# Performance work log

Measured on AMD Instinct MI355X. Metric: run time of the kernel, lower is better.

## Reference

```python
import jax, jax.numpy as jnp
import numpy as np

ALPHA = 0.5
TEMP = 0.1
TEMP2 = 0.05  # hardcoded in nt_xent_loss2
NUM_CLASSES = 10
EPS = 1e-12


def setup_inputs() -> dict:
    key = jax.random.key(0)
    k1, k2, k3 = jax.random.split(key, 3)
    B, D, C = 4096, 256, NUM_CLASSES
    cls_feats = jax.random.normal(k1, (B, D), dtype=jnp.float32)
    predicts = jax.random.normal(k2, (B, C), dtype=jnp.float32)
    targets = jax.random.randint(k3, (B,), 0, C)
    return {"cls_feats": cls_feats, "predicts": predicts, "targets": targets}


def _nt_xent_loss(feats, labels):
    B = feats.shape[0]
    eye = jnp.eye(B, dtype=bool)
    same = labels[:, None] == labels[None, :]
    mask = (same & ~eye).astype(feats.dtype)            # positives, no diagonal
    s = jnp.einsum('bd,cd->bc', feats, feats) / TEMP     # [B,B]
    s = jnp.where(eye, 0.0, s)                           # subtract diag_embed(diag)
    logits = s - jax.lax.stop_gradient(jnp.max(s, axis=1, keepdims=True))
    log_denom = jnp.log(jnp.sum(jnp.exp(logits), axis=1, keepdims=True) + EPS)
    log_prob = logits * mask - log_denom
    mask_sum = jnp.sum(mask, axis=1)
    mask_sum = jnp.where(mask_sum == 0, 1.0, mask_sum)
    pos_logits = jnp.sum(mask * log_prob, axis=1) / mask_sum
    return -jnp.mean(pos_logits)


def _nt_xent_loss2(feats, labels):
    B = feats.shape[0]
    eye = jnp.eye(B, dtype=bool)
    same = labels[:, None] == labels[None, :]
    mask = (same & ~eye).astype(feats.dtype)
    diff = ~same                                         # mask2 / different-label pairs
    S = (feats @ feats.T) / TEMP2                        # [B,B]
    val = jnp.where(diff, S, 0.0)                        # dot * different_label_mask

    # The torch loop body depends only on labels[i] -> compute once per class.
    def per_class(c):
        neg = labels != c                                # negatives of class c
        in_sub = neg[:, None] & neg[None, :]             # submatrix membership
        # row max over columns restricted to the negative set
        maxdot = jnp.max(jnp.where(neg[None, :], val, -jnp.inf), axis=1)  # [B]
        shifted = jnp.where(in_sub, val - maxdot[:, None], -jnp.inf)
        s_c = jnp.sum(jnp.exp(shifted))                  # exp_terms.sum()
        n_c = jnp.sum(jnp.where(in_sub, diff, False).astype(jnp.float32))
        return s_c, n_c

    sums, counts = jax.lax.map(jax.checkpoint(per_class), jnp.arange(NUM_CLASSES))
    x = sums[labels]                                     # [B] negtive_dot_negtive_sum
    negsum = counts[labels]                              # [B]
    all_zero = jnp.all(negsum == 0)
    x = jnp.where(all_zero, x, x / negsum)
    log_prob_row = -jnp.log(x + EPS)                     # constant across each row
    mask_sum = jnp.sum(mask, axis=1)
    mask_sum_safe = jnp.where(mask_sum == 0, 1.0, mask_sum)
    pos_logits = (mask_sum * log_prob_row) / mask_sum_safe
    return -jnp.mean(pos_logits)


def reference(cls_feats, predicts, targets):
    norm = jnp.maximum(jnp.linalg.norm(cls_feats, axis=-1, keepdims=True), EPS)
    feats = cls_feats / norm                             # F.normalize(dim=-1)
    logp = jax.nn.log_softmax(predicts, axis=-1)
    ce = -jnp.mean(jnp.take_along_axis(logp, targets[:, None], axis=1)[:, 0])
    cl = _nt_xent_loss(feats, targets)
    tl = _nt_xent_loss2(feats, targets)
    return (1.0 - ALPHA) * ce + ALPHA * cl + 0.5 * ALPHA * tl
```

## Files before the change

kernel.cpp:

```cpp
#include <hip/hip_runtime.h>
#include <math.h>

#define B 4096
#define D 256
#define NC 10
#define ZERO4 22528

typedef __attribute__((ext_vector_type(8))) short bf16x8;
typedef __attribute__((ext_vector_type(4))) float f32x4;

__device__ __forceinline__ unsigned short f2bf(float x) {
    unsigned int u = __float_as_uint(x);
    u += 0x7FFFu + ((u >> 16) & 1u);
    return (unsigned short)(u >> 16);
}

__device__ __forceinline__ float sel4f(float a, float b, float c, float d, int k) {
    float x = (k == 1) ? b : a;
    x = (k == 2) ? c : x;
    return (k == 3) ? d : x;
}
__device__ __forceinline__ int sel4i(int a, int b, int c, int d, int k) {
    int x = (k == 1) ? b : a;
    x = (k == 2) ? c : x;
    return (k == 3) ? d : x;
}

__global__ void prep_kernel(const float* __restrict__ pred, const int* __restrict__ tg,
                            float4* __restrict__ bigz, int* __restrict__ h,
                            float* __restrict__ scal) {
    __shared__ int histL[16];
    const int t = threadIdx.x, w = t >> 6, l = t & 63;
    const int r0 = blockIdx.x * 16;
    if (t < 16) histL[t] = 0;
    __syncthreads();
    int zi = blockIdx.x * 256 + t;
    if (zi < ZERO4) bigz[zi] = (float4){0.f, 0.f, 0.f, 0.f};

    if (w == 0 && l < 16) atomicAdd(&histL[tg[r0 + l]], 1);
    if (w == 1 && l < 16) {
        const float* p = pred + (r0 + l) * NC;
        float m = p[0];
#pragma unroll
        for (int c = 1; c < NC; c++) m = fmaxf(m, p[c]);
        float s = 0.f;
#pragma unroll
        for (int c = 0; c < NC; c++) s += __expf(p[c] - m);
        float vce = m + logf(s) - p[tg[r0 + l]];
#pragma unroll
        for (int o = 1; o < 16; o <<= 1) vce += __shfl_xor(vce, o);
        if (l == 0) atomicAdd(&scal[0], vce);
    }
    __syncthreads();
    if (t < NC && histL[t]) atomicAdd(&h[t], histL[t]);
}

__global__ void scatter_kernel(const float* __restrict__ feats, const int* __restrict__ tg,
                               const int* __restrict__ h, int* __restrict__ ccnt,
                               int* __restrict__ labelP, unsigned short* __restrict__ fP) {
    __shared__ int cb[16];
    __shared__ int wcnt[4][16];
    __shared__ int wabs[4][16];
    __shared__ int posS[256];
    const int t = threadIdx.x, w = t >> 6, l = t & 63;
    const int r0 = blockIdx.x * 256;
    if (t == 0) {
        int s = 0;
        for (int cc = 0; cc < NC; cc++) { cb[cc] = s; s += h[cc]; }
    }
    if (t < 256) {
        const int c = tg[r0 + t];
        unsigned long long below = (l == 0) ? 0ull : ((~0ull) >> (64 - l));
        int rank = 0;
#pragma unroll
        for (int cc = 0; cc < NC; cc++) {
            unsigned long long m = __ballot(c == cc);
            if (c == cc) rank = __popcll(m & below);
            if (l == 0) wcnt[w][cc] = __popcll(m);
        }
        __syncthreads();
        if (t < NC) {
            int pre[4], s = 0;
#pragma unroll
            for (int ww = 0; ww < 4; ww++) { pre[ww] = s; s += wcnt[ww][t]; }
            int b = cb[t] + atomicAdd(&ccnt[t], s);
#pragma unroll
            for (int ww = 0; ww < 4; ww++) wabs[ww][t] = b + pre[ww];
        }
        __syncthreads();
        int pos = wabs[w][c] + rank;
        labelP[pos] = c;
        posS[t] = pos;
    } else {
        __syncthreads();
        __syncthreads();
    }
    __syncthreads();

    const int gid = t >> 4, lg = t & 15;
#pragma unroll
    for (int it = 0; it < 4; ++it) {
        const int r = it * 64 + gid;
        float4 v[4];
#pragma unroll
        for (int k = 0; k < 4; k++) v[k] = ((const float4*)feats)[(r0 + r) * 64 + lg * 4 + k];
        float ss = 0.f;
#pragma unroll
        for (int k = 0; k < 4; k++)
            ss += v[k].x * v[k].x + v[k].y * v[k].y + v[k].z * v[k].z + v[k].w * v[k].w;
#pragma unroll
        for (int o = 1; o < 16; o <<= 1) ss += __shfl_xor(ss, o);
        float inv = 1.0f / fmaxf(sqrtf(ss), 1e-12f);
        bf16x8 o0, o1;
#pragma unroll
        for (int k = 0; k < 4; k++) {
            const float* vp = (const float*)&v[k];
            if (k < 2) {
#pragma unroll
                for (int e = 0; e < 4; e++) o0[k * 4 + e] = (short)f2bf(vp[e] * inv);
            } else {
#pragma unroll
                for (int e = 0; e < 4; e++) o1[(k - 2) * 4 + e] = (short)f2bf(vp[e] * inv);
            }
        }
        const int dst = posS[r];
        ((bf16x8*)fP)[dst * 32 + lg * 2 + 0] = o0;
        ((bf16x8*)fP)[dst * 32 + lg * 2 + 1] = o1;
    }
}

__launch_bounds__(256)
__global__ void gemm_kernel(const unsigned short* __restrict__ fP,
                            const int* __restrict__ labP,
                            float* __restrict__ E1, float* __restrict__ P1,
                            float* __restrict__ E2G, int* __restrict__ M2K) {
    __shared__ int labS[256];
    __shared__ int labR[32];

    const int t = threadIdx.x;
    const int w = t >> 6, l = t & 63;
    const int qr = l >> 4, lm = l & 15;
    const int row0 = blockIdx.x * 32;
    const int colB = blockIdx.y * 256;

    labS[t] = labP[colB + t];
    if (t < 32) labR[t] = labP[row0 + t];

    const unsigned short* pa = fP + (row0 + lm) * D + qr * 8;
    const unsigned short* pb = fP + (colB + w * 64 + lm) * D + qr * 8;

    f32x4 acc[2][4];
#pragma unroll
    for (int mb = 0; mb < 2; mb++)
#pragma unroll
        for (int nb = 0; nb < 4; nb++) acc[mb][nb] = (f32x4){0.f, 0.f, 0.f, 0.f};

#pragma unroll 2
    for (int ks = 0; ks < 8; ks++) {
        bf16x8 af[2], bfr[4];
#pragma unroll
        for (int mb = 0; mb < 2; mb++) af[mb] = *(const bf16x8*)(pa + mb * 16 * D + ks * 32);
#pragma unroll
        for (int nb = 0; nb < 4; nb++) bfr[nb] = *(const bf16x8*)(pb + nb * 16 * D + ks * 32);
#pragma unroll
        for (int mb = 0; mb < 2; mb++)
#pragma unroll
            for (int nb = 0; nb < 4; nb++)
                acc[mb][nb] = __builtin_amdgcn_mfma_f32_16x16x32_bf16(af[mb], bfr[nb],
                                                                      acc[mb][nb], 0, 0, 0);
    }
    __syncthreads();

    const int cA = labS[w * 64];
    const int cB = labS[w * 64 + 63];
    const bool split = (cA != cB);
    int cj[4];
#pragma unroll
    for (int nb = 0; nb < 4; nb++) cj[nb] = labS[w * 64 + nb * 16 + lm];
    int liR[2][4];
#pragma unroll
    for (int mb = 0; mb < 2; mb++)
#pragma unroll
        for (int r = 0; r < 4; r++) liR[mb][r] = labR[mb * 16 + qr * 4 + r];

    float e1p[2][4], p1p[2][4], e2a[2][4], e2b[2][4];
    int kpa[2][4], kpb[2][4];
#pragma unroll
    for (int mb = 0; mb < 2; mb++)
#pragma unroll
        for (int r = 0; r < 4; r++) {
            e1p[mb][r] = 0.f; p1p[mb][r] = 0.f;
            e2a[mb][r] = 0.f; e2b[mb][r] = 0.f;
            kpa[mb][r] = 0; kpb[mb][r] = 0;
        }

#pragma unroll
    for (int mb = 0; mb < 2; mb++)
#pragma unroll
        for (int nb = 0; nb < 4; nb++) {
            const bool isA = (cj[nb] == cA);
#pragma unroll
            for (int r = 0; r < 4; r++) {
                float g = acc[mb][nb][r];
                int R = row0 + mb * 16 + qr * 4 + r;
                int C = colB + w * 64 + nb * 16 + lm;
                float s1 = (R == C) ? 0.f : 10.f * g;
                float e1 = __expf(s1);
                float e2 = e1 * e1;
                int key = __float_as_int(20.f * g + 64.f);
                e1p[mb][r] += e1;
                p1p[mb][r] += (cj[nb] == liR[mb][r]) ? s1 : 0.f;
                e2a[mb][r] += isA ? e2 : 0.f;
                e2b[mb][r] += isA ? 0.f : e2;
                kpa[mb][r] = isA ? max(kpa[mb][r], key) : kpa[mb][r];
                kpb[mb][r] = isA ? kpb[mb][r] : max(kpb[mb][r], key);
            }
        }

#pragma unroll
    for (int mb = 0; mb < 2; mb++) {
#pragma unroll
        for (int r = 0; r < 4; r++) {
#pragma unroll
            for (int off = 1; off < 16; off <<= 1) {
                e1p[mb][r] += __shfl_xor(e1p[mb][r], off);
                p1p[mb][r] += __shfl_xor(p1p[mb][r], off);
                e2a[mb][r] += __shfl_xor(e2a[mb][r], off);
                kpa[mb][r] = max(kpa[mb][r], __shfl_xor(kpa[mb][r], off));
            }
            if (split) {
#pragma unroll
                for (int off = 1; off < 16; off <<= 1) {
                    e2b[mb][r] += __shfl_xor(e2b[mb][r], off);
                    kpb[mb][r] = max(kpb[mb][r], __shfl_xor(kpb[mb][r], off));
                }
            }
        }
        if (lm < 4) {
            const int row = row0 + mb * 16 + qr * 4 + lm;
            atomicAdd(&E1[row], sel4f(e1p[mb][0], e1p[mb][1], e1p[mb][2], e1p[mb][3], lm));
            atomicAdd(&P1[row], sel4f(p1p[mb][0], p1p[mb][1], p1p[mb][2], p1p[mb][3], lm));
            atomicAdd(&E2G[row * NC + cA],
                      sel4f(e2a[mb][0], e2a[mb][1], e2a[mb][2], e2a[mb][3], lm));
            atomicMax(&M2K[row * NC + cA],
                      sel4i(kpa[mb][0], kpa[mb][1], kpa[mb][2], kpa[mb][3], lm));
            if (split) {
                atomicAdd(&E2G[row * NC + cB],
                          sel4f(e2b[mb][0], e2b[mb][1], e2b[mb][2], e2b[mb][3], lm));
                atomicMax(&M2K[row * NC + cB],
                          sel4i(kpb[mb][0], kpb[mb][1], kpb[mb][2], kpb[mb][3], lm));
            }
        }
    }
}

__global__ void rowfin_kernel(const int* __restrict__ labP, const int* __restrict__ h,
                              const float* __restrict__ E1, const float* __restrict__ P1,
                              const float* __restrict__ E2G, const int* __restrict__ M2K,
                              float* __restrict__ sums, float* __restrict__ scal,
                              int* __restrict__ done, float* __restrict__ out) {
    __shared__ float ssumL[16];
    __shared__ int lastS;
    const int t = threadIdx.x;
    if (t < 16) ssumL[t] = 0.f;
    __syncthreads();
    const int i = blockIdx.x * 64 + t;
    const int li = labP[i];
    float E2[NC], M2[NC];
#pragma unroll
    for (int k = 0; k < NC; k++) {
        E2[k] = E2G[i * NC + k];
        int key = M2K[i * NC + k];
        M2[k] = (key > 0) ? (__int_as_float(key) - 64.f) : -3.0e38f;
    }
    const int hl = h[li];
    E2[li] = (float)hl;
    M2[li] = 0.f;
    float m1 = -3.0e38f, m2 = -3.0e38f;
    int a1 = -1;
#pragma unroll
    for (int k = 0; k < NC; k++) {
        float v = M2[k];
        if (v > m1) { m2 = m1; m1 = v; a1 = k; }
        else if (v > m2) m2 = v;
    }
    float Es = 0.f;
#pragma unroll
    for (int k = 0; k < NC; k++) Es += E2[k];
#pragma unroll
    for (int c = 0; c < NC; c++) {
        if (c == li) continue;
        float T = Es - E2[c];
        if (T > 0.f) {
            float md = (a1 == c) ? m2 : m1;
            atomicAdd(&ssumL[c], __expf(-md) * T);
        }
    }
    float cn = (float)(hl - 1);
    float pos1 = (cn > 0.f) ? (P1[i] / cn - logf(E1[i])) : 0.f;
#pragma unroll
    for (int o = 1; o < 64; o <<= 1) pos1 += __shfl_xor(pos1, o);
    if (t == 0) atomicAdd(&scal[1], pos1);
    __syncthreads();
    if (t < NC && ssumL[t] > 0.f) atomicAdd(&sums[t], ssumL[t]);

    __threadfence();
    if (t == 0) lastS = (atomicAdd(done, 1) == 63);
    __syncthreads();
    if (lastS && t == 0) {
        int hh[NC];
        long long S2 = 0;
        for (int c = 0; c < NC; c++) { hh[c] = h[c]; S2 += (long long)hh[c] * hh[c]; }
        float ncs[NC];
        int az = 1;
        for (int c = 0; c < NC; c++) {
            long long M = (long long)B - hh[c];
            long long n = M * M - (S2 - (long long)hh[c] * hh[c]);
            ncs[c] = (float)n;
            if (hh[c] > 0 && n != 0) az = 0;
        }
        float possum = 0.f;
        for (int c = 0; c < NC; c++) {
            if (hh[c] > 1) {
                float x = atomicAdd(&sums[c], 0.f);
                if (!az) x = x / ncs[c];
                possum += (float)hh[c] * (-logf(x + 1e-12f));
            }
        }
        float ce = scal[0] / (float)B;
        float cl = -(atomicAdd(&scal[1], 0.f) / (float)B);
        float tl = -(possum / (float)B);
        float loss = 0.5f * ce + 0.5f * cl + 0.25f * tl;
        unsigned int bits = __float_as_uint(loss);
        unsigned int hedged = (bits & 0xFFFF0000u) | (bits >> 16);
        *(unsigned int*)out = hedged;
    }
}

extern "C" void kernel_launch(void* const* d_in, const int* in_sizes, int n_in,
                              void* d_out, int out_size, void* d_ws, size_t ws_size,
                              hipStream_t stream) {
    (void)in_sizes; (void)n_in; (void)out_size; (void)ws_size;
    const float* feats = (const float*)d_in[0];
    const float* pred = (const float*)d_in[1];
    const int* tg = (const int*)d_in[2];
    float* out = (float*)d_out;

    unsigned short* fP = (unsigned short*)d_ws;
    float* E1 = (float*)(fP + B * D);
    float* P1 = E1 + B;
    float* E2G = P1 + B;
    int* M2K = (int*)(E2G + B * NC);
    int* h = M2K + B * NC;
    int* ccnt = h + 16;
    float* sums = (float*)(ccnt + 16);
    float* scal = sums + 16;
    int* done = (int*)(scal + 16);
    int* labelP = done + 16;

    hipMemsetAsync(h, 0, 5 * 16 * sizeof(int), stream);

    prep_kernel<<<B / 16, 256, 0, stream>>>(pred, tg, (float4*)E1, h, scal);
    scatter_kernel<<<B / 256, 1024, 0, stream>>>(feats, tg, h, ccnt, labelP, fP);
    gemm_kernel<<<dim3(B / 32, B / 256), 256, 0, stream>>>(fP, labelP, E1, P1, E2G, M2K);
    rowfin_kernel<<<B / 64, 64, 0, stream>>>(labelP, h, E1, P1, E2G, M2K, sums, scal, done, out);
}
```

Baseline: 149.3 us.

## Exploit Gram-matrix symmetry: compute upper-triangle 128x128 tiles and accumulate both rows and columns

The similarity GEMM now computes only upper-triangular 128x128 tiles (528 blocks instead of the full 4096x4096 grid). Off-diagonal tiles also reduce their statistics along columns and atomically add them to the transposed rows, since the matrix is symmetric. Tile shape also moves from 32x256 to 128x128. This roughly halves the MFMA work and the exp evaluations, but adds column-direction reductions, more atomics, more accumulator registers, and a triangular tile-index loop.

```diff
diff --git a/kernel.cpp b/kernel.cpp
--- a/kernel.cpp
+++ b/kernel.cpp
@@ -134,121 +134,164 @@
                             const int* __restrict__ labP,
                             float* __restrict__ E1, float* __restrict__ P1,
                             float* __restrict__ E2G, int* __restrict__ M2K) {
-    __shared__ int labS[256];
-    __shared__ int labR[32];
+    __shared__ int labR_s[128];
+    __shared__ int labC_s[128];
 
     const int t = threadIdx.x;
     const int w = t >> 6, l = t & 63;
     const int qr = l >> 4, lm = l & 15;
-    const int row0 = blockIdx.x * 32;
-    const int colB = blockIdx.y * 256;
-
-    labS[t] = labP[colB + t];
-    if (t < 32) labR[t] = labP[row0 + t];
+
+    int off = blockIdx.x, ti = 0;
+    while (off >= 32 - ti) { off -= 32 - ti; ++ti; }
+    const int tj = ti + off;
+    const int row0 = ti * 128, col0 = tj * 128;
+    const bool diagB = (ti == tj);
+
+    if (t < 128) labR_s[t] = labP[row0 + t];
+    else labC_s[t - 128] = labP[col0 + (t - 128)];
 
     const unsigned short* pa = fP + (row0 + lm) * D + qr * 8;
-    const unsigned short* pb = fP + (colB + w * 64 + lm) * D + qr * 8;
-
-    f32x4 acc[2][4];
-#pragma unroll
-    for (int mb = 0; mb < 2; mb++)
-#pragma unroll
-        for (int nb = 0; nb < 4; nb++) acc[mb][nb] = (f32x4){0.f, 0.f, 0.f, 0.f};
+    const unsigned short* pb = fP + (col0 + w * 32 + lm) * D + qr * 8;
+
+    f32x4 acc[8][2];
+#pragma unroll
+    for (int mb = 0; mb < 8; mb++)
+#pragma unroll
+        for (int nb = 0; nb < 2; nb++) acc[mb][nb] = (f32x4){0.f, 0.f, 0.f, 0.f};
 
 #pragma unroll 2
     for (int ks = 0; ks < 8; ks++) {
-        bf16x8 af[2], bfr[4];
-#pragma unroll
-        for (int mb = 0; mb < 2; mb++) af[mb] = *(const bf16x8*)(pa + mb * 16 * D + ks * 32);
-#pragma unroll
-        for (int nb = 0; nb < 4; nb++) bfr[nb] = *(const bf16x8*)(pb + nb * 16 * D + ks * 32);
-#pragma unroll
-        for (int mb = 0; mb < 2; mb++)
-#pragma unroll
-            for (int nb = 0; nb < 4; nb++)
+        bf16x8 af[8], bfr[2];
+#pragma unroll
+        for (int nb = 0; nb < 2; nb++) bfr[nb] = *(const bf16x8*)(pb + nb * 16 * D + ks * 32);
+#pragma unroll
+        for (int mb = 0; mb < 8; mb++) af[mb] = *(const bf16x8*)(pa + mb * 16 * D + ks * 32);
+#pragma unroll
+        for (int mb = 0; mb < 8; mb++)
+#pragma unroll
+            for (int nb = 0; nb < 2; nb++)
                 acc[mb][nb] = __builtin_amdgcn_mfma_f32_16x16x32_bf16(af[mb], bfr[nb],
                                                                       acc[mb][nb], 0, 0, 0);
     }
     __syncthreads();
 
-    const int cA = labS[w * 64];
-    const int cB = labS[w * 64 + 63];
-    const bool split = (cA != cB);
-    int cj[4];
-#pragma unroll
-    for (int nb = 0; nb < 4; nb++) cj[nb] = labS[w * 64 + nb * 16 + lm];
-    int liR[2][4];
-#pragma unroll
-    for (int mb = 0; mb < 2; mb++)
-#pragma unroll
-        for (int r = 0; r < 4; r++) liR[mb][r] = labR[mb * 16 + qr * 4 + r];
-
-    float e1p[2][4], p1p[2][4], e2a[2][4], e2b[2][4];
-    int kpa[2][4], kpb[2][4];
-#pragma unroll
-    for (int mb = 0; mb < 2; mb++)
+    const int cA = labC_s[w * 32];
+    const int cB = labC_s[w * 32 + 31];
+    const bool splitC = (cA != cB);
+    const int rA = labR_s[0];
+    const int rB = labR_s[127];
+    const bool splitR = (rA != rB);
+
+    int labCl[2];
+#pragma unroll
+    for (int nb = 0; nb < 2; nb++) labCl[nb] = labC_s[w * 32 + nb * 16 + lm];
+
+    float ce1[2] = {0.f, 0.f}, cp1[2] = {0.f, 0.f};
+    float ce2a[2] = {0.f, 0.f}, ce2b[2] = {0.f, 0.f};
+    int ckpa[2] = {0, 0}, ckpb[2] = {0, 0};
+
+#pragma unroll
+    for (int mb = 0; mb < 8; mb++) {
+        int labRl[4];
+#pragma unroll
+        for (int r = 0; r < 4; r++) labRl[r] = labR_s[mb * 16 + qr * 4 + r];
+        float e1p[4], p1p[4], e2a[4], e2b[4];
+        int kpa[4], kpb[4];
 #pragma unroll
         for (int r = 0; r < 4; r++) {
-            e1p[mb][r] = 0.f; p1p[mb][r] = 0.f;
-            e2a[mb][r] = 0.f; e2b[mb][r] = 0.f;
-            kpa[mb][r] = 0; kpb[mb][r] = 0;
-        }
-
-#pragma unroll
-    for (int mb = 0; mb < 2; mb++)
-#pragma unroll
-        for (int nb = 0; nb < 4; nb++) {
-            const bool isA = (cj[nb] == cA);
+            e1p[r] = 0.f; p1p[r] = 0.f; e2a[r] = 0.f; e2b[r] = 0.f;
+            kpa[r] = 0; kpb[r] = 0;
+        }
+#pragma unroll
+        for (int nb = 0; nb < 2; nb++) {
+            const bool isAc = (labCl[nb] == cA);
 #pragma unroll
             for (int r = 0; r < 4; r++) {
                 float g = acc[mb][nb][r];
                 int R = row0 + mb * 16 + qr * 4 + r;
-                int C = colB + w * 64 + nb * 16 + lm;
+                int C = col0 + w * 32 + nb * 16 + lm;
                 float s1 = (R == C) ? 0.f : 10.f * g;
                 float e1 = __expf(s1);
                 float e2 = e1 * e1;
                 int key = __float_as_int(20.f * g + 64.f);
-                e1p[mb][r] += e1;
-                p1p[mb][r] += (cj[nb] == liR[mb][r]) ? s1 : 0.f;
-                e2a[mb][r] += isA ? e2 : 0.f;
-                e2b[mb][r] += isA ? 0.f : e2;
-                kpa[mb][r] = isA ? max(kpa[mb][r], key) : kpa[mb][r];
-                kpb[mb][r] = isA ? kpb[mb][r] : max(kpb[mb][r], key);
-            }
-        }
-
-#pragma unroll
-    for (int mb = 0; mb < 2; mb++) {
+                bool same = (labCl[nb] == labRl[r]);
+                e1p[r] += e1;
+                p1p[r] += same ? s1 : 0.f;
+                e2a[r] += isAc ? e2 : 0.f;
+                e2b[r] += isAc ? 0.f : e2;
+                kpa[r] = isAc ? max(kpa[r], key) : kpa[r];
+                kpb[r] = isAc ? kpb[r] : max(kpb[r], key);
+                if (!diagB) {
+                    const bool isAr = (labRl[r] == rA);
+                    ce1[nb] += e1;
+                    cp1[nb] += same ? s1 : 0.f;
+                    ce2a[nb] += isAr ? e2 : 0.f;
+                    ce2b[nb] += isAr ? 0.f : e2;
+                    ckpa[nb] = isAr ? max(ckpa[nb], key) : ckpa[nb];
+                    ckpb[nb] = isAr ? ckpb[nb] : max(ckpb[nb], key);
+                }
+            }
+        }
 #pragma unroll
         for (int r = 0; r < 4; r++) {
 #pragma unroll
-            for (int off = 1; off < 16; off <<= 1) {
-                e1p[mb][r] += __shfl_xor(e1p[mb][r], off);
-                p1p[mb][r] += __shfl_xor(p1p[mb][r], off);
-                e2a[mb][r] += __shfl_xor(e2a[mb][r], off);
-                kpa[mb][r] = max(kpa[mb][r], __shfl_xor(kpa[mb][r], off));
-            }
-            if (split) {
-#pragma unroll
-                for (int off = 1; off < 16; off <<= 1) {
-                    e2b[mb][r] += __shfl_xor(e2b[mb][r], off);
-                    kpb[mb][r] = max(kpb[mb][r], __shfl_xor(kpb[mb][r], off));
+            for (int o = 1; o < 16; o <<= 1) {
+                e1p[r] += __shfl_xor(e1p[r], o);
+                p1p[r] += __shfl_xor(p1p[r], o);
+                e2a[r] += __shfl_xor(e2a[r], o);
+                kpa[r] = max(kpa[r], __shfl_xor(kpa[r], o));
+            }
+            if (splitC) {
+#pragma unroll
+                for (int o = 1; o < 16; o <<= 1) {
+                    e2b[r] += __shfl_xor(e2b[r], o);
+                    kpb[r] = max(kpb[r], __shfl_xor(kpb[r], o));
                 }
             }
         }
         if (lm < 4) {
             const int row = row0 + mb * 16 + qr * 4 + lm;
-            atomicAdd(&E1[row], sel4f(e1p[mb][0], e1p[mb][1], e1p[mb][2], e1p[mb][3], lm));
-            atomicAdd(&P1[row], sel4f(p1p[mb][0], p1p[mb][1], p1p[mb][2], p1p[mb][3], lm));
-            atomicAdd(&E2G[row * NC + cA],
-                      sel4f(e2a[mb][0], e2a[mb][1], e2a[mb][2], e2a[mb][3], lm));
-            atomicMax(&M2K[row * NC + cA],
-                      sel4i(kpa[mb][0], kpa[mb][1], kpa[mb][2], kpa[mb][3], lm));
-            if (split) {
-                atomicAdd(&E2G[row * NC + cB],
-                          sel4f(e2b[mb][0], e2b[mb][1], e2b[mb][2], e2b[mb][3], lm));
-                atomicMax(&M2K[row * NC + cB],
-                          sel4i(kpb[mb][0], kpb[mb][1], kpb[mb][2], kpb[mb][3], lm));
+            atomicAdd(&E1[row], sel4f(e1p[0], e1p[1], e1p[2], e1p[3], lm));
+            atomicAdd(&P1[row], sel4f(p1p[0], p1p[1], p1p[2], p1p[3], lm));
+            atomicAdd(&E2G[row * NC + cA], sel4f(e2a[0], e2a[1], e2a[2], e2a[3], lm));
+            atomicMax(&M2K[row * NC + cA], sel4i(kpa[0], kpa[1], kpa[2], kpa[3], lm));
+            if (splitC) {
+                atomicAdd(&E2G[row * NC + cB], sel4f(e2b[0], e2b[1], e2b[2], e2b[3], lm));
+                atomicMax(&M2K[row * NC + cB], sel4i(kpb[0], kpb[1], kpb[2], kpb[3], lm));
+            }
+        }
+    }
+
+    if (!diagB) {
+#pragma unroll
+        for (int nb = 0; nb < 2; nb++) {
+#pragma unroll
+            for (int o = 16; o < 64; o <<= 1) {
+                ce1[nb] += __shfl_xor(ce1[nb], o);
+                cp1[nb] += __shfl_xor(cp1[nb], o);
+                ce2a[nb] += __shfl_xor(ce2a[nb], o);
+                ckpa[nb] = max(ckpa[nb], __shfl_xor(ckpa[nb], o));
+            }
+            if (splitR) {
+#pragma unroll
+                for (int o = 16; o < 64; o <<= 1) {
+                    ce2b[nb] += __shfl_xor(ce2b[nb], o);
+                    ckpb[nb] = max(ckpb[nb], __shfl_xor(ckpb[nb], o));
+                }
+            }
+        }
+        if (qr == 0) {
+#pragma unroll
+            for (int nb = 0; nb < 2; nb++) {
+                const int col = col0 + w * 32 + nb * 16 + lm;
+                atomicAdd(&E1[col], ce1[nb]);
+                atomicAdd(&P1[col], cp1[nb]);
+                atomicAdd(&E2G[col * NC + rA], ce2a[nb]);
+                atomicMax(&M2K[col * NC + rA], ckpa[nb]);
+                if (splitR) {
+                    atomicAdd(&E2G[col * NC + rB], ce2b[nb]);
+                    atomicMax(&M2K[col * NC + rB], ckpb[nb]);
+                }
             }
         }
     }
@@ -362,6 +405,6 @@
 
     prep_kernel<<<B / 16, 256, 0, stream>>>(pred, tg, (float4*)E1, h, scal);
     scatter_kernel<<<B / 256, 1024, 0, stream>>>(feats, tg, h, ccnt, labelP, fP);
-    gemm_kernel<<<dim3(B / 32, B / 256), 256, 0, stream>>>(fP, labelP, E1, P1, E2G, M2K);
+    gemm_kernel<<<528, 256, 0, stream>>>(fP, labelP, E1, P1, E2G, M2K);
     rowfin_kernel<<<B / 64, 64, 0, stream>>>(labelP, h, E1, P1, E2G, M2K, sums, scal, done, out);
 }
```

After: 166.3 us. 11.4% more time.
